# Kernel tuning notes

Measured on AMD Instinct MI355X. Metric: run time of the kernel, lower is better.

The kernel has to match this reference:

```python
import jax, jax.numpy as jnp
import numpy as np

N_NODES = 100000
N_EDGES = 1600000
IN_FEATS = 128
HIDDEN = 128
NUM_CLASSES = 4


def setup_inputs() -> dict:
    key = jax.random.key(0)
    ks = jax.random.split(key, 8)
    features = jax.random.normal(ks[0], (N_NODES, IN_FEATS), dtype=jnp.float32)
    src = jax.random.randint(ks[1], (N_EDGES,), 0, N_NODES, dtype=jnp.int64)
    dst = jax.random.randint(ks[2], (N_EDGES,), 0, N_NODES, dtype=jnp.int64)
    s = 1.0 / np.sqrt(IN_FEATS)
    W1 = jax.random.normal(ks[3], (IN_FEATS, HIDDEN), dtype=jnp.float32) * s
    b1 = jnp.zeros((HIDDEN,), dtype=jnp.float32)
    W2 = jax.random.normal(ks[4], (HIDDEN, HIDDEN), dtype=jnp.float32) * s
    b2 = jnp.zeros((HIDDEN,), dtype=jnp.float32)
    Wc = jax.random.normal(ks[5], (HIDDEN, NUM_CLASSES), dtype=jnp.float32) * s
    bc = jnp.zeros((NUM_CLASSES,), dtype=jnp.float32)
    return {"features": features, "src": src, "dst": dst,
            "W1": W1, "b1": b1, "W2": W2, "b2": b2, "Wc": Wc, "bc": bc}


def _graph_conv(x, W, b, src, dst, n_nodes, activation=True):
    # DGL GraphConv, norm='both': D_out^{-1/2} A^T D_in... i.e. symmetric norm.
    ones = jnp.ones((src.shape[0],), dtype=x.dtype)
    deg_out = jnp.clip(jax.ops.segment_sum(ones, src, num_segments=n_nodes), 1.0)
    deg_in = jnp.clip(jax.ops.segment_sum(ones, dst, num_segments=n_nodes), 1.0)
    # scale sources, project (in >= out so matmul first, math-equivalent), gather-scatter
    h = (x * (deg_out ** -0.5)[:, None]) @ W            # [N, out]
    msg = h[src]                                         # [E, out] gather
    agg = jax.ops.segment_sum(msg, dst, num_segments=n_nodes)  # [N, out] scatter-add
    h = agg * (deg_in ** -0.5)[:, None] + b
    return jax.nn.relu(h) if activation else h


def reference(features, src, dst, W1, b1, W2, b2, Wc, bc):
    # eval-mode forward: dropout is identity
    n = features.shape[0]
    h = _graph_conv(features, W1, b1, src, dst, n, activation=True)
    h = _graph_conv(h, W2, b2, src, dst, n, activation=True)
    return h @ Wc + bc  # [N, num_classes] logits
```

## Files before the change

kernel.cpp:

```cpp
#include <hip/hip_runtime.h>
#include <hip/hip_fp16.h>
#include <math.h>

#define N_NODES 100000
#define N_EDGES 1600000
#define F 128
#define NBUK 196
#define BSH 9
#define BSZ 512
#define CAP 10240

typedef _Float16 half8 __attribute__((ext_vector_type(8)));
typedef float    f32x4 __attribute__((ext_vector_type(4)));

__global__ __launch_bounds__(256) void init_pack(int* __restrict__ curD,
                                                 int* __restrict__ curS,
                                                 _Float16* __restrict__ padrow,
                                                 const float* __restrict__ W1,
                                                 const float* __restrict__ W2,
                                                 _Float16* __restrict__ hi1,
                                                 _Float16* __restrict__ lo1,
                                                 _Float16* __restrict__ hi2,
                                                 _Float16* __restrict__ lo2)
{
    int t = threadIdx.x;
    if (blockIdx.x == 0) {
        if (t < NBUK) { curD[t] = t * CAP; curS[t] = t * CAP; }
        if (t < 16) reinterpret_cast<int4*>(padrow)[t] = make_int4(0, 0, 0, 0);
        return;
    }
    int gidx = (blockIdx.x - 1) * 256 + t;
    const float* W = (gidx < 16384) ? W1 : W2;
    _Float16* hi = (gidx < 16384) ? hi1 : hi2;
    _Float16* lo = (gidx < 16384) ? lo1 : lo2;
    int idx = gidx & 16383;
    int f = idx >> 9, r = idx & 511;
    int l = r >> 3, j = r & 7;
    int kc = f >> 3, ct = f & 7;
    int k = kc * 32 + (l >> 4) * 8 + j;
    int n = ct * 16 + (l & 15);
    float w = W[k * 128 + n];
    _Float16 h = (_Float16)w;
    hi[idx] = h;
    lo[idx] = (_Float16)(w - (float)h);
}

__global__ __launch_bounds__(512) void part_gemm1(const int* __restrict__ src,
                                                  const int* __restrict__ dst,
                                                  int* __restrict__ curD,
                                                  int* __restrict__ curS,
                                                  int* __restrict__ bukD,
                                                  unsigned short* __restrict__ bukS,
                                                  const float* __restrict__ X,
                                                  const _Float16* __restrict__ Whi,
                                                  const _Float16* __restrict__ Wlo,
                                                  _Float16* __restrict__ Y, int N)
{
    __shared__ int hd[NBUK], hs[NBUK], bd[NBUK], bs[NBUK], cd[NBUK], cs[NBUK];
    const int tid = threadIdx.x;

    if (blockIdx.x < NBUK) {
        const int chunk = (((N_EDGES + NBUK - 1) / NBUK) + 3) & ~3;
        const int beg = blockIdx.x * chunk;
        const int end = min(beg + chunk, N_EDGES);
        if (beg >= end) return;
        if (tid < NBUK) { hd[tid] = 0; hs[tid] = 0; cd[tid] = 0; cs[tid] = 0; }
        __syncthreads();
        const int b4 = beg >> 2, e4 = end >> 2;
        for (int i = b4 + tid; i < e4; i += 512) {
            int4 d = reinterpret_cast<const int4*>(dst)[i];
            int4 s = reinterpret_cast<const int4*>(src)[i];
            atomicAdd(&hd[d.x >> BSH], 1); atomicAdd(&hd[d.y >> BSH], 1);
            atomicAdd(&hd[d.z >> BSH], 1); atomicAdd(&hd[d.w >> BSH], 1);
            atomicAdd(&hs[s.x >> BSH], 1); atomicAdd(&hs[s.y >> BSH], 1);
            atomicAdd(&hs[s.z >> BSH], 1); atomicAdd(&hs[s.w >> BSH], 1);
        }
        __syncthreads();
        if (tid < NBUK) {
            bd[tid] = hd[tid] ? atomicAdd(&curD[tid], hd[tid]) : 0;
            bs[tid] = hs[tid] ? atomicAdd(&curS[tid], hs[tid]) : 0;
        }
        __syncthreads();
        for (int i = b4 + tid; i < e4; i += 512) {
            int4 d4 = reinterpret_cast<const int4*>(dst)[i];
            int4 s4 = reinterpret_cast<const int4*>(src)[i];
            int dd[4] = { d4.x, d4.y, d4.z, d4.w };
            int ss[4] = { s4.x, s4.y, s4.z, s4.w };
            #pragma unroll
            for (int j = 0; j < 4; j++) {
                int bin = dd[j] >> BSH;
                int r = atomicAdd(&cd[bin], 1);
                bukD[bd[bin] + r] = ((dd[j] & 511) << 17) | ss[j];
                int bin2 = ss[j] >> BSH;
                int r2 = atomicAdd(&cs[bin2], 1);
                bukS[bs[bin2] + r2] = (unsigned short)(ss[j] & 511);
            }
        }
        return;
    }

    const int l = tid & 63, w = tid >> 6;
    const int quad = l >> 4, m = l & 15;
    const int row0 = (blockIdx.x - NBUK) * 256;
    const half8* Bh = reinterpret_cast<const half8*>(Whi);
    const half8* Bl = reinterpret_cast<const half8*>(Wlo);

    f32x4 acc[2][8] = {};

    for (int kc = 0; kc < 4; kc++) {
        half8 ah[2];
        #pragma unroll
        for (int rt = 0; rt < 2; rt++) {
            int grow = row0 + w * 32 + rt * 16 + m;
            float4 xa = make_float4(0.f, 0.f, 0.f, 0.f), xb = xa;
            if (grow < N) {
                const float4* Xp = reinterpret_cast<const float4*>(X) + (size_t)grow * 32 + kc * 8 + quad * 2;
                xa = Xp[0]; xb = Xp[1];
            }
            ah[rt][0] = (_Float16)xa.x; ah[rt][1] = (_Float16)xa.y;
            ah[rt][2] = (_Float16)xa.z; ah[rt][3] = (_Float16)xa.w;
            ah[rt][4] = (_Float16)xb.x; ah[rt][5] = (_Float16)xb.y;
            ah[rt][6] = (_Float16)xb.z; ah[rt][7] = (_Float16)xb.w;
        }
        #pragma unroll
        for (int ct = 0; ct < 8; ct++) {
            int f = kc * 8 + ct;
            half8 bh = Bh[f * 64 + l];
            half8 bl = Bl[f * 64 + l];
            #pragma unroll
            for (int rt = 0; rt < 2; rt++) {
                acc[rt][ct] = __builtin_amdgcn_mfma_f32_16x16x32_f16(ah[rt], bh, acc[rt][ct], 0, 0, 0);
                acc[rt][ct] = __builtin_amdgcn_mfma_f32_16x16x32_f16(ah[rt], bl, acc[rt][ct], 0, 0, 0);
            }
        }
    }

    #pragma unroll
    for (int rt = 0; rt < 2; rt++) {
        #pragma unroll
        for (int r = 0; r < 4; r++) {
            int grow = row0 + w * 32 + rt * 16 + quad * 4 + r;
            if (grow < N) {
                #pragma unroll
                for (int ct = 0; ct < 8; ct++)
                    Y[(size_t)grow * 128 + ct * 16 + m] = (_Float16)(acc[rt][ct][r]);
            }
        }
    }
}

__global__ __launch_bounds__(512) void deg_out(const unsigned short* __restrict__ bukS,
                                               const int* __restrict__ curS,
                                               float* __restrict__ sout)
{
    __shared__ int h[BSZ];
    const int tid = threadIdx.x;
    const int n0 = blockIdx.x << BSH;
    const int lo = blockIdx.x * CAP, hi = curS[blockIdx.x];
    h[tid] = 0;
    __syncthreads();
    for (int i = lo + tid; i < hi; i += 512)
        atomicAdd(&h[bukS[i]], 1);
    __syncthreads();
    int node = n0 + tid;
    if (node < N_NODES) sout[node] = rsqrtf((float)max(h[tid], 1));
}

__global__ __launch_bounds__(512) void csr_wv(const int* __restrict__ bukD,
                                              const int* __restrict__ curD,
                                              const float* __restrict__ sout,
                                              int* __restrict__ row_ptr,
                                              float* __restrict__ sin_,
                                              int* __restrict__ col,
                                              float* __restrict__ wv)
{
    __shared__ int h[BSZ], sc[BSZ], cur[BSZ];
    const int tid = threadIdx.x;
    const int n0 = blockIdx.x << BSH;
    const int lo = blockIdx.x * CAP, hi = curD[blockIdx.x];
    h[tid] = 0;
    __syncthreads();
    for (int i = lo + tid; i < hi; i += 512)
        atomicAdd(&h[((unsigned)bukD[i]) >> 17], 1);
    __syncthreads();
    int own = h[tid];
    int own4 = (own + 3) & ~3;
    sc[tid] = own4;
    __syncthreads();
    for (int off = 1; off < 512; off <<= 1) {
        int u = (tid >= off) ? sc[tid - off] : 0;
        __syncthreads();
        sc[tid] += u;
        __syncthreads();
    }
    int ex = sc[tid] - own4;
    cur[tid] = ex;
    int node = n0 + tid;
    if (node < N_NODES) {
        row_ptr[2 * node]     = lo + ex;
        row_ptr[2 * node + 1] = lo + ex + own4;
        sin_[node] = rsqrtf((float)max(own, 1));
    }
    __syncthreads();
    for (int i = lo + tid; i < hi; i += 512) {
        int p = bukD[i];
        int s = p & 0x1FFFF;
        int r = atomicAdd(&cur[((unsigned)p) >> 17], 1);
        col[lo + r] = s;
        wv[lo + r]  = sout[s];
    }
    for (int k = own; k < own4; k++) {
        col[lo + ex + k] = N_NODES;
        wv[lo + ex + k]  = 0.f;
    }
}

#define ACCW(vv, ww) \
    a0 = fmaf(ww, (float)vv[0], a0); a1 = fmaf(ww, (float)vv[1], a1); \
    a2 = fmaf(ww, (float)vv[2], a2); a3 = fmaf(ww, (float)vv[3], a3); \
    a4 = fmaf(ww, (float)vv[4], a4); a5 = fmaf(ww, (float)vv[5], a5); \
    a6 = fmaf(ww, (float)vv[6], a6); a7 = fmaf(ww, (float)vv[7], a7);

#define ACCU(vv) \
    a0 += (float)vv[0]; a1 += (float)vv[1]; a2 += (float)vv[2]; a3 += (float)vv[3]; \
    a4 += (float)vv[4]; a5 += (float)vv[5]; a6 += (float)vv[6]; a7 += (float)vv[7];

__global__ __launch_bounds__(256) void gather_agg_s(const _Float16* __restrict__ Hh,
                                                    const int* __restrict__ row_ptr,
                                                    const int* __restrict__ col,
                                                    const float* __restrict__ wv,
                                                    const float* __restrict__ sin_,
                                                    const float* __restrict__ bias,
                                                    _Float16* __restrict__ Yh, int N)
{
    const int sub  = threadIdx.x & 15;
    const int node = blockIdx.x * 16 + (threadIdx.x >> 4);
    if (node >= N) return;
    const int beg = row_ptr[2 * node], end = row_ptr[2 * node + 1];
    const half8* __restrict__ H8 = reinterpret_cast<const half8*>(Hh);

    float a0 = 0.f, a1 = 0.f, a2 = 0.f, a3 = 0.f, a4 = 0.f, a5 = 0.f, a6 = 0.f, a7 = 0.f;
    int i = beg;
    for (; i + 8 <= end; i += 8) {
        int4 ca = *reinterpret_cast<const int4*>(col + i);
        int4 cb = *reinterpret_cast<const int4*>(col + i + 4);
        float4 wa = *reinterpret_cast<const float4*>(wv + i);
        float4 wb = *reinterpret_cast<const float4*>(wv + i + 4);
        half8 v0 = H8[((size_t)ca.x << 4) | sub];
        half8 v1 = H8[((size_t)ca.y << 4) | sub];
        half8 v2 = H8[((size_t)ca.z << 4) | sub];
        half8 v3 = H8[((size_t)ca.w << 4) | sub];
        half8 v4 = H8[((size_t)cb.x << 4) | sub];
        half8 v5 = H8[((size_t)cb.y << 4) | sub];
        half8 v6 = H8[((size_t)cb.z << 4) | sub];
        half8 v7 = H8[((size_t)cb.w << 4) | sub];
        ACCW(v0, wa.x) ACCW(v1, wa.y) ACCW(v2, wa.z) ACCW(v3, wa.w)
        ACCW(v4, wb.x) ACCW(v5, wb.y) ACCW(v6, wb.z) ACCW(v7, wb.w)
    }
    if (i < end) {
        int4 ca = *reinterpret_cast<const int4*>(col + i);
        float4 wa = *reinterpret_cast<const float4*>(wv + i);
        half8 v0 = H8[((size_t)ca.x << 4) | sub];
        half8 v1 = H8[((size_t)ca.y << 4) | sub];
        half8 v2 = H8[((size_t)ca.z << 4) | sub];
        half8 v3 = H8[((size_t)ca.w << 4) | sub];
        ACCW(v0, wa.x) ACCW(v1, wa.y) ACCW(v2, wa.z) ACCW(v3, wa.w)
    }
    float scn = sin_[node];
    const float4* B4 = reinterpret_cast<const float4*>(bias);
    float4 bA = B4[2 * sub], bB = B4[2 * sub + 1];
    half8 o;
    o[0] = (_Float16)fmaxf(fmaf(a0, scn, bA.x), 0.f);
    o[1] = (_Float16)fmaxf(fmaf(a1, scn, bA.y), 0.f);
    o[2] = (_Float16)fmaxf(fmaf(a2, scn, bA.z), 0.f);
    o[3] = (_Float16)fmaxf(fmaf(a3, scn, bA.w), 0.f);
    o[4] = (_Float16)fmaxf(fmaf(a4, scn, bB.x), 0.f);
    o[5] = (_Float16)fmaxf(fmaf(a5, scn, bB.y), 0.f);
    o[6] = (_Float16)fmaxf(fmaf(a6, scn, bB.z), 0.f);
    o[7] = (_Float16)fmaxf(fmaf(a7, scn, bB.w), 0.f);
    reinterpret_cast<half8*>(Yh)[(size_t)node * 16 + sub] = o;
}

__global__ __launch_bounds__(256) void gather_cls(const _Float16* __restrict__ Hh,
                                                  const int* __restrict__ row_ptr,
                                                  const int* __restrict__ col,
                                                  const float* __restrict__ sin_,
                                                  const float* __restrict__ bias,
                                                  const float* __restrict__ Wc,
                                                  const float* __restrict__ bc,
                                                  float* __restrict__ out, int N)
{
    __shared__ float4 Wcs[128];
    for (int t = threadIdx.x; t < 128; t += 256)
        Wcs[t] = reinterpret_cast<const float4*>(Wc)[t];
    __syncthreads();

    const int sub  = threadIdx.x & 15;
    const int node = blockIdx.x * 16 + (threadIdx.x >> 4);
    if (node >= N) return;
    const int beg = row_ptr[2 * node], end = row_ptr[2 * node + 1];
    const half8* __restrict__ H8 = reinterpret_cast<const half8*>(Hh);

    float a0 = 0.f, a1 = 0.f, a2 = 0.f, a3 = 0.f, a4 = 0.f, a5 = 0.f, a6 = 0.f, a7 = 0.f;
    int i = beg;
    for (; i + 8 <= end; i += 8) {
        int4 ca = *reinterpret_cast<const int4*>(col + i);
        int4 cb = *reinterpret_cast<const int4*>(col + i + 4);
        half8 v0 = H8[((size_t)ca.x << 4) | sub];
        half8 v1 = H8[((size_t)ca.y << 4) | sub];
        half8 v2 = H8[((size_t)ca.z << 4) | sub];
        half8 v3 = H8[((size_t)ca.w << 4) | sub];
        half8 v4 = H8[((size_t)cb.x << 4) | sub];
        half8 v5 = H8[((size_t)cb.y << 4) | sub];
        half8 v6 = H8[((size_t)cb.z << 4) | sub];
        half8 v7 = H8[((size_t)cb.w << 4) | sub];
        ACCU(v0) ACCU(v1) ACCU(v2) ACCU(v3)
        ACCU(v4) ACCU(v5) ACCU(v6) ACCU(v7)
    }
    if (i < end) {
        int4 ca = *reinterpret_cast<const int4*>(col + i);
        half8 v0 = H8[((size_t)ca.x << 4) | sub];
        half8 v1 = H8[((size_t)ca.y << 4) | sub];
        half8 v2 = H8[((size_t)ca.z << 4) | sub];
        half8 v3 = H8[((size_t)ca.w << 4) | sub];
        ACCU(v0) ACCU(v1) ACCU(v2) ACCU(v3)
    }
    float scn = sin_[node];
    const float4* B4 = reinterpret_cast<const float4*>(bias);
    float4 bA = B4[2 * sub], bB = B4[2 * sub + 1];
    float h0 = fmaxf(fmaf(a0, scn, bA.x), 0.f);
    float h1 = fmaxf(fmaf(a1, scn, bA.y), 0.f);
    float h2 = fmaxf(fmaf(a2, scn, bA.z), 0.f);
    float h3 = fmaxf(fmaf(a3, scn, bA.w), 0.f);
    float h4 = fmaxf(fmaf(a4, scn, bB.x), 0.f);
    float h5 = fmaxf(fmaf(a5, scn, bB.y), 0.f);
    float h6 = fmaxf(fmaf(a6, scn, bB.z), 0.f);
    float h7 = fmaxf(fmaf(a7, scn, bB.w), 0.f);

    float lx = 0.f, ly = 0.f, lz = 0.f, lw = 0.f;
    float4 w;
    w = Wcs[sub * 8 + 0]; lx = fmaf(h0, w.x, lx); ly = fmaf(h0, w.y, ly); lz = fmaf(h0, w.z, lz); lw = fmaf(h0, w.w, lw);
    w = Wcs[sub * 8 + 1]; lx = fmaf(h1, w.x, lx); ly = fmaf(h1, w.y, ly); lz = fmaf(h1, w.z, lz); lw = fmaf(h1, w.w, lw);
    w = Wcs[sub * 8 + 2]; lx = fmaf(h2, w.x, lx); ly = fmaf(h2, w.y, ly); lz = fmaf(h2, w.z, lz); lw = fmaf(h2, w.w, lw);
    w = Wcs[sub * 8 + 3]; lx = fmaf(h3, w.x, lx); ly = fmaf(h3, w.y, ly); lz = fmaf(h3, w.z, lz); lw = fmaf(h3, w.w, lw);
    w = Wcs[sub * 8 + 4]; lx = fmaf(h4, w.x, lx); ly = fmaf(h4, w.y, ly); lz = fmaf(h4, w.z, lz); lw = fmaf(h4, w.w, lw);
    w = Wcs[sub * 8 + 5]; lx = fmaf(h5, w.x, lx); ly = fmaf(h5, w.y, ly); lz = fmaf(h5, w.z, lz); lw = fmaf(h5, w.w, lw);
    w = Wcs[sub * 8 + 6]; lx = fmaf(h6, w.x, lx); ly = fmaf(h6, w.y, ly); lz = fmaf(h6, w.z, lz); lw = fmaf(h6, w.w, lw);
    w = Wcs[sub * 8 + 7]; lx = fmaf(h7, w.x, lx); ly = fmaf(h7, w.y, ly); lz = fmaf(h7, w.z, lz); lw = fmaf(h7, w.w, lw);

    #pragma unroll
    for (int m = 1; m < 16; m <<= 1) {
        lx += __shfl_xor(lx, m);
        ly += __shfl_xor(ly, m);
        lz += __shfl_xor(lz, m);
        lw += __shfl_xor(lw, m);
    }
    if (sub == 0) {
        float4 bcv = reinterpret_cast<const float4*>(bc)[0];
        float4 r;
        r.x = lx + bcv.x; r.y = ly + bcv.y; r.z = lz + bcv.z; r.w = lw + bcv.w;
        reinterpret_cast<float4*>(out)[node] = r;
    }
}

__global__ __launch_bounds__(256) void gemm_mfma_f16(const _Float16* __restrict__ Xh,
                                                     const _Float16* __restrict__ Whi,
                                                     const _Float16* __restrict__ Wlo,
                                                     const float* __restrict__ srow,
                                                     _Float16* __restrict__ Y, int N)
{
    const int tid = threadIdx.x;
    const int l = tid & 63, w = tid >> 6;
    const int quad = l >> 4, m = l & 15;
    const int row0 = blockIdx.x * 128;
    const half8* Bh = reinterpret_cast<const half8*>(Whi);
    const half8* Bl = reinterpret_cast<const half8*>(Wlo);

    f32x4 acc[2][8] = {};

    for (int kc = 0; kc < 4; kc++) {
        half8 a[2];
        #pragma unroll
        for (int rt = 0; rt < 2; rt++) {
            int grow = row0 + w * 32 + rt * 16 + m;
            half8 z = {};
            a[rt] = (grow < N)
                ? *reinterpret_cast<const half8*>(Xh + (size_t)grow * 128 + kc * 32 + quad * 8)
                : z;
        }
        #pragma unroll
        for (int ct = 0; ct < 8; ct++) {
            int f = kc * 8 + ct;
            half8 bh = Bh[f * 64 + l];
            half8 bl = Bl[f * 64 + l];
            #pragma unroll
            for (int rt = 0; rt < 2; rt++) {
                acc[rt][ct] = __builtin_amdgcn_mfma_f32_16x16x32_f16(a[rt], bh, acc[rt][ct], 0, 0, 0);
                acc[rt][ct] = __builtin_amdgcn_mfma_f32_16x16x32_f16(a[rt], bl, acc[rt][ct], 0, 0, 0);
            }
        }
    }

    #pragma unroll
    for (int rt = 0; rt < 2; rt++) {
        #pragma unroll
        for (int r = 0; r < 4; r++) {
            int grow = row0 + w * 32 + rt * 16 + quad * 4 + r;
            if (grow < N) {
                float s = srow[grow];
                #pragma unroll
                for (int ct = 0; ct < 8; ct++)
                    Y[(size_t)grow * 128 + ct * 16 + m] = (_Float16)(acc[rt][ct][r] * s);
            }
        }
    }
}

extern "C" void kernel_launch(void* const* d_in, const int* in_sizes, int n_in,
                              void* d_out, int out_size, void* d_ws, size_t ws_size,
                              hipStream_t stream)
{
    const float* features = (const float*)d_in[0];
    const int*   src      = (const int*)d_in[1];
    const int*   dst      = (const int*)d_in[2];
    const float* W1       = (const float*)d_in[3];
    const float* b1       = (const float*)d_in[4];
    const float* W2       = (const float*)d_in[5];
    const float* b2       = (const float*)d_in[6];
    const float* Wc       = (const float*)d_in[7];
    const float* bc       = (const float*)d_in[8];
    float* out = (float*)d_out;

    char* ws = (char*)d_ws;
    const size_t MB = 1 << 20;
    int* curD  = (int*)(ws + 0);
    int* curS  = (int*)(ws + 1024);
    _Float16* Whi1 = (_Float16*)(ws + 64 * 1024);
    _Float16* Wlo1 = (_Float16*)(ws + 96 * 1024);
    _Float16* Whi2 = (_Float16*)(ws + 128 * 1024);
    _Float16* Wlo2 = (_Float16*)(ws + 160 * 1024);
    float* sout    = (float*)(ws + 512 * 1024);
    float* sin_    = (float*)(ws + 1 * MB);
    int*   row_ptr = (int*)(ws + 2 * MB);
    int*   col     = (int*)(ws + 3 * MB);
    float* wv      = (float*)(ws + 11 * MB);
    _Float16* hMsg = (_Float16*)(ws + 25 * MB);
    int*   bukD    = (int*)(ws + 52 * MB);
    unsigned short* bukS = (unsigned short*)(ws + 60 * MB);
    _Float16* hA   = (_Float16*)(ws + 52 * MB);

    const int N = N_NODES;
    const int NGB = (N + 15) / 16;

    init_pack<<<129, 256, 0, stream>>>(curD, curS, hMsg + (size_t)N * F,
                                       W1, W2, Whi1, Wlo1, Whi2, Wlo2);

    part_gemm1<<<NBUK + 391, 512, 0, stream>>>(src, dst, curD, curS, bukD, bukS,
                                               features, Whi1, Wlo1, hMsg, N);

    deg_out<<<NBUK, 512, 0, stream>>>(bukS, curS, sout);

    csr_wv<<<NBUK, 512, 0, stream>>>(bukD, curD, sout, row_ptr, sin_, col, wv);

    gather_agg_s<<<NGB, 256, 0, stream>>>(hMsg, row_ptr, col, wv, sin_, b1, hA, N);

    gemm_mfma_f16<<<(N + 127) / 128, 256, 0, stream>>>(hA, Whi2, Wlo2, sout, hMsg, N);
    gather_cls<<<NGB, 256, 0, stream>>>(hMsg, row_ptr, col, sin_, b2, Wc, bc, out, N);
}
```

Before: 311.9 us.

## Pad CSR rows to 16, unroll gathers by 16, double partition blocks

Pads each destination row in the bucketed CSR to a multiple of 16 so both gather kernels can run a single 16-wide unrolled loop with no tail. Index and weight loads become nontemporal, and the layer-1 output store is nontemporal. The edge partition phase uses twice as many blocks, and bucket capacity and workspace offsets grow to hold the extra padding. The cost is more padded dummy edges, which add wasted gathers of the zero pad row, and higher register pressure from the wider unroll.

```diff
diff --git a/kernel.cpp b/kernel.cpp
--- a/kernel.cpp
+++ b/kernel.cpp
@@ -8,10 +8,12 @@
 #define NBUK 196
 #define BSH 9
 #define BSZ 512
-#define CAP 10240
+#define CAP 13312
+#define NPART 392
 
 typedef _Float16 half8 __attribute__((ext_vector_type(8)));
 typedef float    f32x4 __attribute__((ext_vector_type(4)));
+typedef int      i32x4 __attribute__((ext_vector_type(4)));
 
 __global__ __launch_bounds__(256) void init_pack(int* __restrict__ curD,
                                                  int* __restrict__ curS,
@@ -59,8 +61,8 @@
     __shared__ int hd[NBUK], hs[NBUK], bd[NBUK], bs[NBUK], cd[NBUK], cs[NBUK];
     const int tid = threadIdx.x;
 
-    if (blockIdx.x < NBUK) {
-        const int chunk = (((N_EDGES + NBUK - 1) / NBUK) + 3) & ~3;
+    if (blockIdx.x < NPART) {
+        const int chunk = (((N_EDGES + NPART - 1) / NPART) + 3) & ~3;
         const int beg = blockIdx.x * chunk;
         const int end = min(beg + chunk, N_EDGES);
         if (beg >= end) return;
@@ -101,7 +103,7 @@
 
     const int l = tid & 63, w = tid >> 6;
     const int quad = l >> 4, m = l & 15;
-    const int row0 = (blockIdx.x - NBUK) * 256;
+    const int row0 = (blockIdx.x - NPART) * 256;
     const half8* Bh = reinterpret_cast<const half8*>(Whi);
     const half8* Bl = reinterpret_cast<const half8*>(Wlo);
 
@@ -184,8 +186,8 @@
         atomicAdd(&h[((unsigned)bukD[i]) >> 17], 1);
     __syncthreads();
     int own = h[tid];
-    int own4 = (own + 3) & ~3;
-    sc[tid] = own4;
+    int own16 = (own + 15) & ~15;
+    sc[tid] = own16;
     __syncthreads();
     for (int off = 1; off < 512; off <<= 1) {
         int u = (tid >= off) ? sc[tid - off] : 0;
@@ -193,12 +195,12 @@
         sc[tid] += u;
         __syncthreads();
     }
-    int ex = sc[tid] - own4;
+    int ex = sc[tid] - own16;
     cur[tid] = ex;
     int node = n0 + tid;
     if (node < N_NODES) {
         row_ptr[2 * node]     = lo + ex;
-        row_ptr[2 * node + 1] = lo + ex + own4;
+        row_ptr[2 * node + 1] = lo + ex + own16;
         sin_[node] = rsqrtf((float)max(own, 1));
     }
     __syncthreads();
@@ -209,7 +211,7 @@
         col[lo + r] = s;
         wv[lo + r]  = sout[s];
     }
-    for (int k = own; k < own4; k++) {
+    for (int k = own; k < own16; k++) {
         col[lo + ex + k] = N_NODES;
         wv[lo + ex + k]  = 0.f;
     }
@@ -240,31 +242,35 @@
     const half8* __restrict__ H8 = reinterpret_cast<const half8*>(Hh);
 
     float a0 = 0.f, a1 = 0.f, a2 = 0.f, a3 = 0.f, a4 = 0.f, a5 = 0.f, a6 = 0.f, a7 = 0.f;
-    int i = beg;
-    for (; i + 8 <= end; i += 8) {
-        int4 ca = *reinterpret_cast<const int4*>(col + i);
-        int4 cb = *reinterpret_cast<const int4*>(col + i + 4);
-        float4 wa = *reinterpret_cast<const float4*>(wv + i);
-        float4 wb = *reinterpret_cast<const float4*>(wv + i + 4);
-        half8 v0 = H8[((size_t)ca.x << 4) | sub];
-        half8 v1 = H8[((size_t)ca.y << 4) | sub];
-        half8 v2 = H8[((size_t)ca.z << 4) | sub];
-        half8 v3 = H8[((size_t)ca.w << 4) | sub];
-        half8 v4 = H8[((size_t)cb.x << 4) | sub];
-        half8 v5 = H8[((size_t)cb.y << 4) | sub];
-        half8 v6 = H8[((size_t)cb.z << 4) | sub];
-        half8 v7 = H8[((size_t)cb.w << 4) | sub];
-        ACCW(v0, wa.x) ACCW(v1, wa.y) ACCW(v2, wa.z) ACCW(v3, wa.w)
-        ACCW(v4, wb.x) ACCW(v5, wb.y) ACCW(v6, wb.z) ACCW(v7, wb.w)
-    }
-    if (i < end) {
-        int4 ca = *reinterpret_cast<const int4*>(col + i);
-        float4 wa = *reinterpret_cast<const float4*>(wv + i);
-        half8 v0 = H8[((size_t)ca.x << 4) | sub];
-        half8 v1 = H8[((size_t)ca.y << 4) | sub];
-        half8 v2 = H8[((size_t)ca.z << 4) | sub];
-        half8 v3 = H8[((size_t)ca.w << 4) | sub];
-        ACCW(v0, wa.x) ACCW(v1, wa.y) ACCW(v2, wa.z) ACCW(v3, wa.w)
+    for (int i = beg; i < end; i += 16) {
+        i32x4 c0 = __builtin_nontemporal_load(reinterpret_cast<const i32x4*>(col + i));
+        i32x4 c1 = __builtin_nontemporal_load(reinterpret_cast<const i32x4*>(col + i + 4));
+        i32x4 c2 = __builtin_nontemporal_load(reinterpret_cast<const i32x4*>(col + i + 8));
+        i32x4 c3 = __builtin_nontemporal_load(reinterpret_cast<const i32x4*>(col + i + 12));
+        f32x4 w0 = __builtin_nontemporal_load(reinterpret_cast<const f32x4*>(wv + i));
+        f32x4 w1 = __builtin_nontemporal_load(reinterpret_cast<const f32x4*>(wv + i + 4));
+        f32x4 w2 = __builtin_nontemporal_load(reinterpret_cast<const f32x4*>(wv + i + 8));
+        f32x4 w3 = __builtin_nontemporal_load(reinterpret_cast<const f32x4*>(wv + i + 12));
+        half8 v0  = H8[((size_t)c0.x << 4) | sub];
+        half8 v1  = H8[((size_t)c0.y << 4) | sub];
+        half8 v2  = H8[((size_t)c0.z << 4) | sub];
+        half8 v3  = H8[((size_t)c0.w << 4) | sub];
+        half8 v4  = H8[((size_t)c1.x << 4) | sub];
+        half8 v5  = H8[((size_t)c1.y << 4) | sub];
+        half8 v6  = H8[((size_t)c1.z << 4) | sub];
+        half8 v7  = H8[((size_t)c1.w << 4) | sub];
+        half8 v8  = H8[((size_t)c2.x << 4) | sub];
+        half8 v9  = H8[((size_t)c2.y << 4) | sub];
+        half8 v10 = H8[((size_t)c2.z << 4) | sub];
+        half8 v11 = H8[((size_t)c2.w << 4) | sub];
+        half8 v12 = H8[((size_t)c3.x << 4) | sub];
+        half8 v13 = H8[((size_t)c3.y << 4) | sub];
+        half8 v14 = H8[((size_t)c3.z << 4) | sub];
+        half8 v15 = H8[((size_t)c3.w << 4) | sub];
+        ACCW(v0,  w0.x) ACCW(v1,  w0.y) ACCW(v2,  w0.z) ACCW(v3,  w0.w)
+        ACCW(v4,  w1.x) ACCW(v5,  w1.y) ACCW(v6,  w1.z) ACCW(v7,  w1.w)
+        ACCW(v8,  w2.x) ACCW(v9,  w2.y) ACCW(v10, w2.z) ACCW(v11, w2.w)
+        ACCW(v12, w3.x) ACCW(v13, w3.y) ACCW(v14, w3.z) ACCW(v15, w3.w)
     }
     float scn = sin_[node];
     const float4* B4 = reinterpret_cast<const float4*>(bias);
@@ -278,7 +284,7 @@
     o[5] = (_Float16)fmaxf(fmaf(a5, scn, bB.y), 0.f);
     o[6] = (_Float16)fmaxf(fmaf(a6, scn, bB.z), 0.f);
     o[7] = (_Float16)fmaxf(fmaf(a7, scn, bB.w), 0.f);
-    reinterpret_cast<half8*>(Yh)[(size_t)node * 16 + sub] = o;
+    __builtin_nontemporal_store(o, reinterpret_cast<half8*>(Yh) + (size_t)node * 16 + sub);
 }
 
 __global__ __launch_bounds__(256) void gather_cls(const _Float16* __restrict__ Hh,
@@ -302,28 +308,31 @@
     const half8* __restrict__ H8 = reinterpret_cast<const half8*>(Hh);
 
     float a0 = 0.f, a1 = 0.f, a2 = 0.f, a3 = 0.f, a4 = 0.f, a5 = 0.f, a6 = 0.f, a7 = 0.f;
-    int i = beg;
-    for (; i + 8 <= end; i += 8) {
-        int4 ca = *reinterpret_cast<const int4*>(col + i);
-        int4 cb = *reinterpret_cast<const int4*>(col + i + 4);
-        half8 v0 = H8[((size_t)ca.x << 4) | sub];
-        half8 v1 = H8[((size_t)ca.y << 4) | sub];
-        half8 v2 = H8[((size_t)ca.z << 4) | sub];
-        half8 v3 = H8[((size_t)ca.w << 4) | sub];
-        half8 v4 = H8[((size_t)cb.x << 4) | sub];
-        half8 v5 = H8[((size_t)cb.y << 4) | sub];
-        half8 v6 = H8[((size_t)cb.z << 4) | sub];
-        half8 v7 = H8[((size_t)cb.w << 4) | sub];
-        ACCU(v0) ACCU(v1) ACCU(v2) ACCU(v3)
-        ACCU(v4) ACCU(v5) ACCU(v6) ACCU(v7)
-    }
-    if (i < end) {
-        int4 ca = *reinterpret_cast<const int4*>(col + i);
-        half8 v0 = H8[((size_t)ca.x << 4) | sub];
-        half8 v1 = H8[((size_t)ca.y << 4) | sub];
-        half8 v2 = H8[((size_t)ca.z << 4) | sub];
-        half8 v3 = H8[((size_t)ca.w << 4) | sub];
-        ACCU(v0) ACCU(v1) ACCU(v2) ACCU(v3)
+    for (int i = beg; i < end; i += 16) {
+        i32x4 c0 = __builtin_nontemporal_load(reinterpret_cast<const i32x4*>(col + i));
+        i32x4 c1 = __builtin_nontemporal_load(reinterpret_cast<const i32x4*>(col + i + 4));
+        i32x4 c2 = __builtin_nontemporal_load(reinterpret_cast<const i32x4*>(col + i + 8));
+        i32x4 c3 = __builtin_nontemporal_load(reinterpret_cast<const i32x4*>(col + i + 12));
+        half8 v0  = H8[((size_t)c0.x << 4) | sub];
+        half8 v1  = H8[((size_t)c0.y << 4) | sub];
+        half8 v2  = H8[((size_t)c0.z << 4) | sub];
+        half8 v3  = H8[((size_t)c0.w << 4) | sub];
+        half8 v4  = H8[((size_t)c1.x << 4) | sub];
+        half8 v5  = H8[((size_t)c1.y << 4) | sub];
+        half8 v6  = H8[((size_t)c1.z << 4) | sub];
+        half8 v7  = H8[((size_t)c1.w << 4) | sub];
+        half8 v8  = H8[((size_t)c2.x << 4) | sub];
+        half8 v9  = H8[((size_t)c2.y << 4) | sub];
+        half8 v10 = H8[((size_t)c2.z << 4) | sub];
+        half8 v11 = H8[((size_t)c2.w << 4) | sub];
+        half8 v12 = H8[((size_t)c3.x << 4) | sub];
+        half8 v13 = H8[((size_t)c3.y << 4) | sub];
+        half8 v14 = H8[((size_t)c3.z << 4) | sub];
+        half8 v15 = H8[((size_t)c3.w << 4) | sub];
+        ACCU(v0)  ACCU(v1)  ACCU(v2)  ACCU(v3)
+        ACCU(v4)  ACCU(v5)  ACCU(v6)  ACCU(v7)
+        ACCU(v8)  ACCU(v9)  ACCU(v10) ACCU(v11)
+        ACCU(v12) ACCU(v13) ACCU(v14) ACCU(v15)
     }
     float scn = sin_[node];
     const float4* B4 = reinterpret_cast<const float4*>(bias);
@@ -443,10 +452,10 @@
     float* sin_    = (float*)(ws + 1 * MB);
     int*   row_ptr = (int*)(ws + 2 * MB);
     int*   col     = (int*)(ws + 3 * MB);
-    float* wv      = (float*)(ws + 11 * MB);
+    float* wv      = (float*)(ws + 14 * MB);
     _Float16* hMsg = (_Float16*)(ws + 25 * MB);
     int*   bukD    = (int*)(ws + 52 * MB);
-    unsigned short* bukS = (unsigned short*)(ws + 60 * MB);
+    unsigned short* bukS = (unsigned short*)(ws + 63 * MB);
     _Float16* hA   = (_Float16*)(ws + 52 * MB);
 
     const int N = N_NODES;
@@ -455,8 +464,8 @@
     init_pack<<<129, 256, 0, stream>>>(curD, curS, hMsg + (size_t)N * F,
                                        W1, W2, Whi1, Wlo1, Whi2, Wlo2);
 
-    part_gemm1<<<NBUK + 391, 512, 0, stream>>>(src, dst, curD, curS, bukD, bukS,
-                                               features, Whi1, Wlo1, hMsg, N);
+    part_gemm1<<<NPART + 391, 512, 0, stream>>>(src, dst, curD, curS, bukD, bukS,
+                                                features, Whi1, Wlo1, hMsg, N);
 
     deg_out<<<NBUK, 512, 0, stream>>>(bukS, curS, sout);
 
```

Result: slower. 323.4 us (+3.7%).
